# Kernel optimization log

Measured on AMD Instinct MI355X. Metric: run time of the kernel, lower is better.

The kernel has to match this reference:

```python
import jax, jax.numpy as jnp
import numpy as np
from jax import lax

ALPHA = 1.5
N_ITER = 100


def entmax(z, alpha=ALPHA, n_iter=N_ITER):
    # z: [B, Sq, Sk] scores. Bisection for the entmax threshold tau.
    z = (alpha - 1.0) * z.astype(jnp.float32)
    S = z.shape[-1]
    z_max = jnp.max(z, axis=-1, keepdims=True)          # [B, Sq, 1]
    tau_min = z_max - 1.0
    tau_max = z_max - np.float32(S ** (1.0 - alpha))
    inv = 1.0 / (alpha - 1.0)                            # = 2.0 for alpha=1.5

    def body(carry, _):
        tmin, tmax, _ = carry
        tau = (tmin + tmax) * 0.5
        p = jnp.maximum(z - tau, 0.0) ** inv             # [B, Sq, Sk]
        Z = jnp.sum(p, axis=-1, keepdims=True)           # [B, Sq, 1]
        tmin = jnp.where(Z >= 1.0, tau, tmin)
        tmax = jnp.where(Z < 1.0, tau, tmax)
        return (tmin, tmax, tau), None

    init = (tau_min, tau_max, (tau_min + tau_max) * 0.5)
    (tmin, tmax, tau), _ = lax.scan(jax.checkpoint(body), init, None, length=n_iter)
    # faithful to the TF code: final output uses p, Z from the LAST iteration's tau
    p = jnp.maximum(z - tau, 0.0) ** inv
    Z = jnp.sum(p, axis=-1, keepdims=True)
    return p / Z


def setup_inputs() -> dict:
    key = jax.random.key(0)
    kq, kk, kv = jax.random.split(key, 3)
    B, S, D = 8, 2048, 128
    return {
        "query": jax.random.normal(kq, (B, S, D), dtype=jnp.float32),
        "key": jax.random.normal(kk, (B, S, D), dtype=jnp.float32),
        "value": jax.random.normal(kv, (B, S, D), dtype=jnp.float32),
    }


def reference(query, key, value):
    scores = jnp.einsum("bqd,bkd->bqk", query, key)      # QK^T, no scaling (as in source)
    weights = entmax(scores, alpha=ALPHA, n_iter=N_ITER)
    return jnp.einsum("bqk,bkd->bqd", weights, value)
```

## Files before the change

kernel.cpp:

```cpp
#include <hip/hip_runtime.h>

#define BB 8
#define SS 2048
#define DD 128
#define ROWS 16
#define NW 8
#define CTW 16

typedef short bf16x8 __attribute__((ext_vector_type(8)));
typedef float f32x4 __attribute__((ext_vector_type(4)));

template <int I> struct IC { static constexpr int value = I; };
template <int I, int N, typename F>
__device__ __forceinline__ void sfor(F&& f) {
  if constexpr (I < N) { f(IC<I>{}); sfor<I + 1, N>((F&&)f); }
}

__device__ __forceinline__ short f2bf(float x) {
  return __builtin_bit_cast(short, (__bf16)x);
}
__device__ __forceinline__ float bf2f(short u) {
  return __uint_as_float(((unsigned)(unsigned short)u) << 16);
}
__device__ __forceinline__ unsigned pk2(float a, float b) {
  return (unsigned)(unsigned short)f2bf(a) |
         ((unsigned)(unsigned short)f2bf(b) << 16);
}

template <int N> __device__ __forceinline__ void wait_vm() {
  if constexpr (N >= 6)      asm volatile("s_waitcnt vmcnt(6)" ::: "memory");
  else if constexpr (N == 5) asm volatile("s_waitcnt vmcnt(5)" ::: "memory");
  else if constexpr (N == 4) asm volatile("s_waitcnt vmcnt(4)" ::: "memory");
  else if constexpr (N == 3) asm volatile("s_waitcnt vmcnt(3)" ::: "memory");
  else if constexpr (N == 2) asm volatile("s_waitcnt vmcnt(2)" ::: "memory");
  else if constexpr (N == 1) asm volatile("s_waitcnt vmcnt(1)" ::: "memory");
  else                       asm volatile("s_waitcnt vmcnt(0)" ::: "memory");
}

__device__ __forceinline__ void stage1(const short* g, short* l) {
  __builtin_amdgcn_global_load_lds(
      (const __attribute__((address_space(1))) void*)g,
      (__attribute__((address_space(3))) void*)l, 16, 0, 0);
}

__global__ __launch_bounds__(256)
void ksplit(const float* __restrict__ K, short* __restrict__ Khi) {
  const int lin  = blockIdx.x * 256 + threadIdx.x;
  const int b    = lin >> 15;
  const int rem  = lin & 32767;
  const int ct   = rem >> 8;
  const int s    = (rem >> 6) & 3;
  const int lane = rem & 63;
  const int quad = lane >> 4, m16 = lane & 15;
  const size_t elem = (size_t)(b * SS + ct * 16 + m16) * DD + s * 32 + quad * 8;
  const float4 v0 = *(const float4*)(K + elem);
  const float4 v1 = *(const float4*)(K + elem + 4);
  const float f[8] = {v0.x, v0.y, v0.z, v0.w, v1.x, v1.y, v1.z, v1.w};
  bf16x8 h;
#pragma unroll
  for (int e = 0; e < 8; ++e) h[e] = f2bf(f[e]);
  *(bf16x8*)(Khi + (size_t)lin * 8) = h;
}

__global__ __launch_bounds__(512) __attribute__((amdgpu_waves_per_eu(4)))
void attn(const float* __restrict__ Q, const short* __restrict__ Khi,
          const float* __restrict__ K, const float* __restrict__ V,
          float* __restrict__ Out) {
  __shared__ short kring[NW][8][512];
  __shared__ unsigned short Qs[ROWS][136];
  __shared__ float rbuf[ROWS][64];
  __shared__ int   scol[ROWS][64];
  __shared__ float exM[NW][ROWS];
  __shared__ int   rcnt[ROWS];
  __shared__ int   rovf[ROWS];
  __shared__ float tauB[ROWS], ZB[ROWS];

  const int tid  = threadIdx.x;
  const int lane = tid & 63;
  const int wid  = __builtin_amdgcn_readfirstlane(tid >> 6);
  const int quad = lane >> 4, m16 = lane & 15;
  const int b    = blockIdx.x & 7;
  const int qt   = blockIdx.x >> 3;

  const float* Qb = Q + (size_t)(b * SS + qt * ROWS) * DD;
  const float* Kb = K + (size_t)b * SS * DD;
  const float* Vb = V + (size_t)b * SS * DD;
  float*       Ob = Out + (size_t)(b * SS + qt * ROWS) * DD;
  const short* KHb = Khi + (size_t)b * SS * DD;

  if (tid < ROWS) { rcnt[tid] = 0; rovf[tid] = 0; }

  {
    const int row = tid >> 5, d = (tid & 31) * 4;
    const float4 v = *(const float4*)&Qb[row * DD + d];
    ushort4 h;
    h.x = (unsigned short)f2bf(0.5f * v.x);
    h.y = (unsigned short)f2bf(0.5f * v.y);
    h.z = (unsigned short)f2bf(0.5f * v.z);
    h.w = (unsigned short)f2bf(0.5f * v.w);
    *(ushort4*)&Qs[row][d] = h;
  }
  __syncthreads();

  bf16x8 qh[4];
#pragma unroll
  for (int s = 0; s < 4; ++s)
    qh[s] = *(const bf16x8*)&Qs[m16][s * 32 + quad * 8];

  short* ring = &kring[wid][0][0];
  const short* gw = KHb + ((size_t)(wid * CTW) << 11) + lane * 8;

  sfor<0, 7>([&](auto pc) {
    constexpr int p = pc.value;
    stage1(gw + p * 512, ring + p * 512);
  });

  unsigned zpk[CTW][2];
  float mx[4] = {-1e38f, -1e38f, -1e38f, -1e38f};
  f32x4 acc = {0.f, 0.f, 0.f, 0.f};

  sfor<0, 64>([&](auto qc) {
    constexpr int q = qc.value;
    wait_vm<(63 - q < 6 ? 63 - q : 6)>();
    asm volatile("s_waitcnt lgkmcnt(0)" ::: "memory");
    if constexpr (q + 7 < 64)
      stage1(gw + (q + 7) * 512, ring + ((q + 7) & 7) * 512);
    const bf16x8 bh = *(const bf16x8*)(ring + ((q & 7) << 9) + lane * 8);
    constexpr int s = q & 3;
    if constexpr (s == 0) acc = f32x4{0.f, 0.f, 0.f, 0.f};
    acc = __builtin_amdgcn_mfma_f32_16x16x32_bf16(qh[s], bh, acc, 0, 0, 0);
    if constexpr (s == 3) {
      constexpr int ct = q >> 2;
#pragma unroll
      for (int j = 0; j < 4; ++j) mx[j] = fmaxf(mx[j], acc[j]);
      zpk[ct][0] = pk2(acc[0], acc[1]);
      zpk[ct][1] = pk2(acc[2], acc[3]);
    }
  });

#pragma unroll
  for (int j = 0; j < 4; ++j)
#pragma unroll
    for (int s = 1; s <= 8; s <<= 1) mx[j] = fmaxf(mx[j], __shfl_xor(mx[j], s));
  if (m16 == 0) {
#pragma unroll
    for (int j = 0; j < 4; ++j) exM[wid][4 * quad + j] = mx[j];
  }
  __syncthreads();
  float M4[4];
#pragma unroll
  for (int j = 0; j < 4; ++j) {
    float m = -1e38f;
#pragma unroll
    for (int w = 0; w < NW; ++w) m = fmaxf(m, exM[w][4 * quad + j]);
    M4[j] = m;
  }

  sfor<0, CTW>([&](auto cc) {
    constexpr int ct = cc.value;
    const int col = wid * 256 + ct * 16 + m16;
    float v[4];
    v[0] = __uint_as_float(zpk[ct][0] << 16);
    v[1] = __uint_as_float(zpk[ct][0] & 0xffff0000u);
    v[2] = __uint_as_float(zpk[ct][1] << 16);
    v[3] = __uint_as_float(zpk[ct][1] & 0xffff0000u);
#pragma unroll
    for (int j = 0; j < 4; ++j) {
      const int row = 4 * quad + j;
      if (v[j] > M4[j] - 1.35f) {
        const int pos = atomicAdd(&rcnt[row], 1);
        if (pos < 64) { scol[row][pos] = col; rbuf[row][pos] = v[j]; }
        else rovf[row] = 1;
      }
    }
  });
  __syncthreads();

  const int rr32 = lane >> 5;
  const int row  = 2 * wid + rr32;
  const int l32  = lane & 31;
  const int nA = rcnt[2 * wid]     < 64 ? rcnt[2 * wid]     : 64;
  const int nB = rcnt[2 * wid + 1] < 64 ? rcnt[2 * wid + 1] : 64;
  const int nr  = rr32 ? nB : nA;
  const int nmx = nA > nB ? nA : nB;

  {
    const float4 q4 = *(const float4*)&Qb[row * DD + l32 * 4];
    for (int i = 0; i < nmx; ++i) {
      const bool act = i < nr;
      const int c = act ? scol[row][i] : scol[row][0];
      const float4 k4 = *(const float4*)&Kb[(size_t)c * DD + l32 * 4];
      float t = q4.x * k4.x + q4.y * k4.y + q4.z * k4.z + q4.w * k4.w;
#pragma unroll
      for (int s = 1; s <= 16; s <<= 1) t += __shfl_xor(t, s);
      if (act && l32 == 0) rbuf[row][i] = 0.5f * t;
    }
  }

  {
    const float a0 = (l32 < nr)      ? rbuf[row][l32]      : -1e38f;
    const float a1 = (l32 + 32 < nr) ? rbuf[row][l32 + 32] : -1e38f;
    float Mr = fmaxf(a0, a1);
#pragma unroll
    for (int s = 1; s <= 16; s <<= 1) Mr = fmaxf(Mr, __shfl_xor(Mr, s));
    float tmn = Mr - 1.0f, tmx = Mr - 0.022097086912079608f;
    float tau = 0.5f * (tmn + tmx), Zr = 0.f;
    for (int it = 0; it < 100; ++it) {
      tau = 0.5f * (tmn + tmx);
      const float t0 = fmaxf(a0 - tau, 0.f);
      const float t1 = fmaxf(a1 - tau, 0.f);
      float zp = fmaf(t0, t0, t1 * t1);
#pragma unroll
      for (int s = 1; s <= 16; s <<= 1) zp += __shfl_xor(zp, s);
      Zr = zp;
      const float nmn = (zp >= 1.f) ? tau : tmn;
      const float nmx = (zp >= 1.f) ? tmx : tau;
      const bool ch = (nmn != tmn) || (nmx != tmx);
      tmn = nmn; tmx = nmx;
      if (!__any(ch)) break;
    }
    if (l32 == 0) { tauB[row] = tau; ZB[row] = Zr; }
  }

  if (!rovf[row]) {
    const float tau = tauB[row];
    const float iz  = 1.0f / ZB[row];
    float4 o = {0.f, 0.f, 0.f, 0.f};
    for (int i = 0; i < nr; ++i) {
      const float rv = rbuf[row][i];
      const float tt = fmaxf(rv - tau, 0.f);
      const float pi = tt * tt * iz;
      const int   c  = scol[row][i];
      const float4 v4 = *(const float4*)&Vb[(size_t)c * DD + l32 * 4];
      o.x = fmaf(pi, v4.x, o.x);
      o.y = fmaf(pi, v4.y, o.y);
      o.z = fmaf(pi, v4.z, o.z);
      o.w = fmaf(pi, v4.w, o.w);
    }
    *(float4*)&Ob[row * DD + l32 * 4] = o;
  }

#pragma unroll
  for (int rr = 0; rr < 2; ++rr) {
    const int frow = 2 * wid + rr;
    if (!rovf[frow]) continue;
    float* zr = (float*)&kring[wid][0][0];
    for (int c0 = 0; c0 < 32; ++c0) {
      const int c = c0 * 64 + lane;
      const float* kp = &Kb[(size_t)c * DD];
      float t = 0.f;
      for (int d = 0; d < DD; d += 4) {
        const float4 qv = *(const float4*)&Qb[frow * DD + d];
        const float4 kv = *(const float4*)&kp[d];
        t = fmaf(qv.x, kv.x, t); t = fmaf(qv.y, kv.y, t);
        t = fmaf(qv.z, kv.z, t); t = fmaf(qv.w, kv.w, t);
      }
      zr[c] = 0.5f * t;
    }
    float Mr = -1e38f;
    for (int c0 = 0; c0 < 32; ++c0) Mr = fmaxf(Mr, zr[c0 * 64 + lane]);
#pragma unroll
    for (int s = 1; s <= 32; s <<= 1) Mr = fmaxf(Mr, __shfl_xor(Mr, s));
    float tmn = Mr - 1.0f, tmx = Mr - 0.022097086912079608f;
    float tau = 0.5f * (tmn + tmx), Zr = 0.f;
    for (int it = 0; it < 100; ++it) {
      tau = 0.5f * (tmn + tmx);
      float zp = 0.f;
      for (int c0 = 0; c0 < 32; ++c0) {
        const float tt = fmaxf(zr[c0 * 64 + lane] - tau, 0.f);
        zp = fmaf(tt, tt, zp);
      }
#pragma unroll
      for (int s = 1; s <= 32; s <<= 1) zp += __shfl_xor(zp, s);
      Zr = zp;
      const float nmn = (zp >= 1.f) ? tau : tmn;
      const float nmx = (zp >= 1.f) ? tmx : tau;
      const bool ch = (nmn != tmn) || (nmx != tmx);
      tmn = nmn; tmx = nmx;
      if (!__any(ch)) break;
    }
    const float iz = 1.0f / Zr;
    float2 o = {0.f, 0.f};
    for (int c = 0; c < SS; ++c) {
      const float tt = fmaxf(zr[c] - tau, 0.f);
      if (tt > 0.f) {
        const float pi = tt * tt * iz;
        const float2 v2 = *(const float2*)&Vb[(size_t)c * DD + lane * 2];
        o.x = fmaf(pi, v2.x, o.x);
        o.y = fmaf(pi, v2.y, o.y);
      }
    }
    *(float2*)&Ob[frow * DD + lane * 2] = o;
  }
}

extern "C" void kernel_launch(void* const* d_in, const int* in_sizes, int n_in,
                              void* d_out, int out_size, void* d_ws, size_t ws_size,
                              hipStream_t stream) {
  const float* Q = (const float*)d_in[0];
  const float* K = (const float*)d_in[1];
  const float* V = (const float*)d_in[2];
  float* out = (float*)d_out;
  short* Khi = (short*)d_ws;

  hipLaunchKernelGGL(ksplit, dim3(BB * SS * DD / (256 * 8)), dim3(256), 0, stream,
                     K, Khi);
  hipLaunchKernelGGL(attn, dim3(BB * (SS / ROWS)), dim3(512), 0, stream,
                     Q, Khi, K, V, out);
}
```

Before: 128.0 us.

## Process 32 query rows per block, reusing each staged K tile across two MFMA row groups

Doubles the query rows per block from 16 to 32, so each bf16 K tile staged into LDS feeds two MFMA accumulators (two 16-row groups). This halves both the K streaming traffic per output row and the number of blocks. The candidate buffer capacity drops from 64 to 48 per row and shares LDS with the Q staging buffer to limit shared-memory growth. The prefetch depth is also reduced. The trade-offs are fewer blocks for occupancy, more rows falling into the slow full-row overflow fallback, and a more serial per-wave post-processing loop.

```diff
diff --git a/kernel.cpp b/kernel.cpp
--- a/kernel.cpp
+++ b/kernel.cpp
@@ -3,9 +3,10 @@
 #define BB 8
 #define SS 2048
 #define DD 128
-#define ROWS 16
+#define ROWS 32
 #define NW 8
 #define CTW 16
+#define CAP 48
 
 typedef short bf16x8 __attribute__((ext_vector_type(8)));
 typedef float f32x4 __attribute__((ext_vector_type(4)));
@@ -18,9 +19,6 @@
 
 __device__ __forceinline__ short f2bf(float x) {
   return __builtin_bit_cast(short, (__bf16)x);
-}
-__device__ __forceinline__ float bf2f(short u) {
-  return __uint_as_float(((unsigned)(unsigned short)u) << 16);
 }
 __device__ __forceinline__ unsigned pk2(float a, float b) {
   return (unsigned)(unsigned short)f2bf(a) |
@@ -67,9 +65,10 @@
           const float* __restrict__ K, const float* __restrict__ V,
           float* __restrict__ Out) {
   __shared__ short kring[NW][8][512];
-  __shared__ unsigned short Qs[ROWS][136];
-  __shared__ float rbuf[ROWS][64];
-  __shared__ int   scol[ROWS][64];
+  __shared__ __align__(16) char ubuf[12288];
+  unsigned short (*Qs)[136] = (unsigned short (*)[136])ubuf;
+  float (*rbuf)[CAP] = (float (*)[CAP])ubuf;
+  int   (*scol)[CAP] = (int (*)[CAP])(ubuf + ROWS * CAP * 4);
   __shared__ float exM[NW][ROWS];
   __shared__ int   rcnt[ROWS];
   __shared__ int   rovf[ROWS];
@@ -91,158 +90,197 @@
   if (tid < ROWS) { rcnt[tid] = 0; rovf[tid] = 0; }
 
   {
-    const int row = tid >> 5, d = (tid & 31) * 4;
-    const float4 v = *(const float4*)&Qb[row * DD + d];
-    ushort4 h;
-    h.x = (unsigned short)f2bf(0.5f * v.x);
-    h.y = (unsigned short)f2bf(0.5f * v.y);
-    h.z = (unsigned short)f2bf(0.5f * v.z);
-    h.w = (unsigned short)f2bf(0.5f * v.w);
-    *(ushort4*)&Qs[row][d] = h;
+    const int row = tid >> 4, d = (tid & 15) * 8;
+    const float4 v0 = *(const float4*)&Qb[row * DD + d];
+    const float4 v1 = *(const float4*)&Qb[row * DD + d + 4];
+    ushort4 h0, h1;
+    h0.x = (unsigned short)f2bf(0.5f * v0.x);
+    h0.y = (unsigned short)f2bf(0.5f * v0.y);
+    h0.z = (unsigned short)f2bf(0.5f * v0.z);
+    h0.w = (unsigned short)f2bf(0.5f * v0.w);
+    h1.x = (unsigned short)f2bf(0.5f * v1.x);
+    h1.y = (unsigned short)f2bf(0.5f * v1.y);
+    h1.z = (unsigned short)f2bf(0.5f * v1.z);
+    h1.w = (unsigned short)f2bf(0.5f * v1.w);
+    *(ushort4*)&Qs[row][d]     = h0;
+    *(ushort4*)&Qs[row][d + 4] = h1;
   }
   __syncthreads();
 
-  bf16x8 qh[4];
-#pragma unroll
-  for (int s = 0; s < 4; ++s)
-    qh[s] = *(const bf16x8*)&Qs[m16][s * 32 + quad * 8];
-
   short* ring = &kring[wid][0][0];
   const short* gw = KHb + ((size_t)(wid * CTW) << 11) + lane * 8;
 
-  sfor<0, 7>([&](auto pc) {
+  sfor<0, 6>([&](auto pc) {
     constexpr int p = pc.value;
     stage1(gw + p * 512, ring + p * 512);
   });
 
-  unsigned zpk[CTW][2];
-  float mx[4] = {-1e38f, -1e38f, -1e38f, -1e38f};
-  f32x4 acc = {0.f, 0.f, 0.f, 0.f};
-
-  sfor<0, 64>([&](auto qc) {
-    constexpr int q = qc.value;
-    wait_vm<(63 - q < 6 ? 63 - q : 6)>();
+  bf16x8 qh[2][4];
+#pragma unroll
+  for (int g = 0; g < 2; ++g)
+#pragma unroll
+    for (int s = 0; s < 4; ++s)
+      qh[g][s] = *(const bf16x8*)&Qs[g * 16 + m16][s * 32 + quad * 8];
+
+  unsigned zpk[2][CTW][2];
+  float mx[2][4] = {{-1e38f, -1e38f, -1e38f, -1e38f},
+                    {-1e38f, -1e38f, -1e38f, -1e38f}};
+  f32x4 accA = {0.f, 0.f, 0.f, 0.f}, accB = {0.f, 0.f, 0.f, 0.f};
+
+  sfor<0, 32>([&](auto ii) {
+    constexpr int i = ii.value;
+    constexpr int left = 62 - 2 * i;
+    wait_vm<(left < 0 ? 0 : (left > 4 ? 4 : left))>();
     asm volatile("s_waitcnt lgkmcnt(0)" ::: "memory");
-    if constexpr (q + 7 < 64)
-      stage1(gw + (q + 7) * 512, ring + ((q + 7) & 7) * 512);
-    const bf16x8 bh = *(const bf16x8*)(ring + ((q & 7) << 9) + lane * 8);
-    constexpr int s = q & 3;
-    if constexpr (s == 0) acc = f32x4{0.f, 0.f, 0.f, 0.f};
-    acc = __builtin_amdgcn_mfma_f32_16x16x32_bf16(qh[s], bh, acc, 0, 0, 0);
-    if constexpr (s == 3) {
-      constexpr int ct = q >> 2;
-#pragma unroll
-      for (int j = 0; j < 4; ++j) mx[j] = fmaxf(mx[j], acc[j]);
-      zpk[ct][0] = pk2(acc[0], acc[1]);
-      zpk[ct][1] = pk2(acc[2], acc[3]);
+    if constexpr (2 * i + 7 < 64) {
+      stage1(gw + (2 * i + 6) * 512, ring + ((2 * i + 6) & 7) * 512);
+      stage1(gw + (2 * i + 7) * 512, ring + ((2 * i + 7) & 7) * 512);
+    }
+    const bf16x8 b0 = *(const bf16x8*)(ring + (((2 * i)     & 7) << 9) + lane * 8);
+    const bf16x8 b1 = *(const bf16x8*)(ring + (((2 * i + 1) & 7) << 9) + lane * 8);
+    constexpr int s0 = (2 * i) & 3;
+    constexpr int s1 = s0 + 1;
+    if constexpr (s0 == 0) {
+      accA = f32x4{0.f, 0.f, 0.f, 0.f};
+      accB = f32x4{0.f, 0.f, 0.f, 0.f};
+    }
+    accA = __builtin_amdgcn_mfma_f32_16x16x32_bf16(qh[0][s0], b0, accA, 0, 0, 0);
+    accB = __builtin_amdgcn_mfma_f32_16x16x32_bf16(qh[1][s0], b0, accB, 0, 0, 0);
+    accA = __builtin_amdgcn_mfma_f32_16x16x32_bf16(qh[0][s1], b1, accA, 0, 0, 0);
+    accB = __builtin_amdgcn_mfma_f32_16x16x32_bf16(qh[1][s1], b1, accB, 0, 0, 0);
+    if constexpr (s1 == 3) {
+      constexpr int ct = i >> 1;
+#pragma unroll
+      for (int j = 0; j < 4; ++j) {
+        mx[0][j] = fmaxf(mx[0][j], accA[j]);
+        mx[1][j] = fmaxf(mx[1][j], accB[j]);
+      }
+      zpk[0][ct][0] = pk2(accA[0], accA[1]);
+      zpk[0][ct][1] = pk2(accA[2], accA[3]);
+      zpk[1][ct][0] = pk2(accB[0], accB[1]);
+      zpk[1][ct][1] = pk2(accB[2], accB[3]);
     }
   });
 
 #pragma unroll
-  for (int j = 0; j < 4; ++j)
-#pragma unroll
-    for (int s = 1; s <= 8; s <<= 1) mx[j] = fmaxf(mx[j], __shfl_xor(mx[j], s));
+  for (int g = 0; g < 2; ++g)
+#pragma unroll
+    for (int j = 0; j < 4; ++j)
+#pragma unroll
+      for (int s = 1; s <= 8; s <<= 1)
+        mx[g][j] = fmaxf(mx[g][j], __shfl_xor(mx[g][j], s));
   if (m16 == 0) {
 #pragma unroll
-    for (int j = 0; j < 4; ++j) exM[wid][4 * quad + j] = mx[j];
+    for (int g = 0; g < 2; ++g)
+#pragma unroll
+      for (int j = 0; j < 4; ++j) exM[wid][g * 16 + 4 * quad + j] = mx[g][j];
   }
   __syncthreads();
-  float M4[4];
-#pragma unroll
-  for (int j = 0; j < 4; ++j) {
-    float m = -1e38f;
-#pragma unroll
-    for (int w = 0; w < NW; ++w) m = fmaxf(m, exM[w][4 * quad + j]);
-    M4[j] = m;
-  }
+  float M4[2][4];
+#pragma unroll
+  for (int g = 0; g < 2; ++g)
+#pragma unroll
+    for (int j = 0; j < 4; ++j) {
+      float m = -1e38f;
+#pragma unroll
+      for (int w = 0; w < NW; ++w) m = fmaxf(m, exM[w][g * 16 + 4 * quad + j]);
+      M4[g][j] = m;
+    }
 
   sfor<0, CTW>([&](auto cc) {
     constexpr int ct = cc.value;
     const int col = wid * 256 + ct * 16 + m16;
-    float v[4];
-    v[0] = __uint_as_float(zpk[ct][0] << 16);
-    v[1] = __uint_as_float(zpk[ct][0] & 0xffff0000u);
-    v[2] = __uint_as_float(zpk[ct][1] << 16);
-    v[3] = __uint_as_float(zpk[ct][1] & 0xffff0000u);
-#pragma unroll
-    for (int j = 0; j < 4; ++j) {
-      const int row = 4 * quad + j;
-      if (v[j] > M4[j] - 1.35f) {
-        const int pos = atomicAdd(&rcnt[row], 1);
-        if (pos < 64) { scol[row][pos] = col; rbuf[row][pos] = v[j]; }
-        else rovf[row] = 1;
+#pragma unroll
+    for (int g = 0; g < 2; ++g) {
+      float v[4];
+      v[0] = __uint_as_float(zpk[g][ct][0] << 16);
+      v[1] = __uint_as_float(zpk[g][ct][0] & 0xffff0000u);
+      v[2] = __uint_as_float(zpk[g][ct][1] << 16);
+      v[3] = __uint_as_float(zpk[g][ct][1] & 0xffff0000u);
+#pragma unroll
+      for (int j = 0; j < 4; ++j) {
+        const int row = g * 16 + 4 * quad + j;
+        if (v[j] > M4[g][j] - 1.35f) {
+          const int pos = atomicAdd(&rcnt[row], 1);
+          if (pos < CAP) { scol[row][pos] = col; rbuf[row][pos] = v[j]; }
+          else rovf[row] = 1;
+        }
       }
     }
   });
   __syncthreads();
 
   const int rr32 = lane >> 5;
-  const int row  = 2 * wid + rr32;
   const int l32  = lane & 31;
-  const int nA = rcnt[2 * wid]     < 64 ? rcnt[2 * wid]     : 64;
-  const int nB = rcnt[2 * wid + 1] < 64 ? rcnt[2 * wid + 1] : 64;
-  const int nr  = rr32 ? nB : nA;
-  const int nmx = nA > nB ? nA : nB;
-
-  {
-    const float4 q4 = *(const float4*)&Qb[row * DD + l32 * 4];
-    for (int i = 0; i < nmx; ++i) {
-      const bool act = i < nr;
-      const int c = act ? scol[row][i] : scol[row][0];
-      const float4 k4 = *(const float4*)&Kb[(size_t)c * DD + l32 * 4];
-      float t = q4.x * k4.x + q4.y * k4.y + q4.z * k4.z + q4.w * k4.w;
-#pragma unroll
-      for (int s = 1; s <= 16; s <<= 1) t += __shfl_xor(t, s);
-      if (act && l32 == 0) rbuf[row][i] = 0.5f * t;
+
+#pragma unroll
+  for (int p = 0; p < 2; ++p) {
+    const int row = 4 * wid + 2 * p + rr32;
+    const int nA = rcnt[4 * wid + 2 * p]     < CAP ? rcnt[4 * wid + 2 * p]     : CAP;
+    const int nB = rcnt[4 * wid + 2 * p + 1] < CAP ? rcnt[4 * wid + 2 * p + 1] : CAP;
+    const int nr  = rr32 ? nB : nA;
+    const int nmx = nA > nB ? nA : nB;
+
+    {
+      const float4 q4 = *(const float4*)&Qb[row * DD + l32 * 4];
+      for (int i = 0; i < nmx; ++i) {
+        const bool act = i < nr;
+        const int c = act ? scol[row][i] : scol[row][0];
+        const float4 k4 = *(const float4*)&Kb[(size_t)c * DD + l32 * 4];
+        float t = q4.x * k4.x + q4.y * k4.y + q4.z * k4.z + q4.w * k4.w;
+#pragma unroll
+        for (int s = 1; s <= 16; s <<= 1) t += __shfl_xor(t, s);
+        if (act && l32 == 0) rbuf[row][i] = 0.5f * t;
+      }
+    }
+
+    {
+      const float a0 = (l32 < nr)      ? rbuf[row][l32]      : -1e38f;
+      const float a1 = (l32 + 32 < nr) ? rbuf[row][l32 + 32] : -1e38f;
+      float Mr = fmaxf(a0, a1);
+#pragma unroll
+      for (int s = 1; s <= 16; s <<= 1) Mr = fmaxf(Mr, __shfl_xor(Mr, s));
+      float tmn = Mr - 1.0f, tmx = Mr - 0.022097086912079608f;
+      float tau = 0.5f * (tmn + tmx), Zr = 0.f;
+      for (int it = 0; it < 100; ++it) {
+        tau = 0.5f * (tmn + tmx);
+        const float t0 = fmaxf(a0 - tau, 0.f);
+        const float t1 = fmaxf(a1 - tau, 0.f);
+        float zp = fmaf(t0, t0, t1 * t1);
+#pragma unroll
+        for (int s = 1; s <= 16; s <<= 1) zp += __shfl_xor(zp, s);
+        Zr = zp;
+        const float nmn = (zp >= 1.f) ? tau : tmn;
+        const float nmx2 = (zp >= 1.f) ? tmx : tau;
+        const bool ch = (nmn != tmn) || (nmx2 != tmx);
+        tmn = nmn; tmx = nmx2;
+        if (!__any(ch)) break;
+      }
+      if (l32 == 0) { tauB[row] = tau; ZB[row] = Zr; }
+    }
+
+    if (!rovf[row]) {
+      const float tau = tauB[row];
+      const float iz  = 1.0f / ZB[row];
+      float4 o = {0.f, 0.f, 0.f, 0.f};
+      for (int i = 0; i < nr; ++i) {
+        const float rv = rbuf[row][i];
+        const float tt = fmaxf(rv - tau, 0.f);
+        const float pi = tt * tt * iz;
+        const int   c  = scol[row][i];
+        const float4 v4 = *(const float4*)&Vb[(size_t)c * DD + l32 * 4];
+        o.x = fmaf(pi, v4.x, o.x);
+        o.y = fmaf(pi, v4.y, o.y);
+        o.z = fmaf(pi, v4.z, o.z);
+        o.w = fmaf(pi, v4.w, o.w);
+      }
+      *(float4*)&Ob[row * DD + l32 * 4] = o;
     }
   }
 
-  {
-    const float a0 = (l32 < nr)      ? rbuf[row][l32]      : -1e38f;
-    const float a1 = (l32 + 32 < nr) ? rbuf[row][l32 + 32] : -1e38f;
-    float Mr = fmaxf(a0, a1);
-#pragma unroll
-    for (int s = 1; s <= 16; s <<= 1) Mr = fmaxf(Mr, __shfl_xor(Mr, s));
-    float tmn = Mr - 1.0f, tmx = Mr - 0.022097086912079608f;
-    float tau = 0.5f * (tmn + tmx), Zr = 0.f;
-    for (int it = 0; it < 100; ++it) {
-      tau = 0.5f * (tmn + tmx);
-      const float t0 = fmaxf(a0 - tau, 0.f);
-      const float t1 = fmaxf(a1 - tau, 0.f);
-      float zp = fmaf(t0, t0, t1 * t1);
-#pragma unroll
-      for (int s = 1; s <= 16; s <<= 1) zp += __shfl_xor(zp, s);
-      Zr = zp;
-      const float nmn = (zp >= 1.f) ? tau : tmn;
-      const float nmx = (zp >= 1.f) ? tmx : tau;
-      const bool ch = (nmn != tmn) || (nmx != tmx);
-      tmn = nmn; tmx = nmx;
-      if (!__any(ch)) break;
-    }
-    if (l32 == 0) { tauB[row] = tau; ZB[row] = Zr; }
-  }
-
-  if (!rovf[row]) {
-    const float tau = tauB[row];
-    const float iz  = 1.0f / ZB[row];
-    float4 o = {0.f, 0.f, 0.f, 0.f};
-    for (int i = 0; i < nr; ++i) {
-      const float rv = rbuf[row][i];
-      const float tt = fmaxf(rv - tau, 0.f);
-      const float pi = tt * tt * iz;
-      const int   c  = scol[row][i];
-      const float4 v4 = *(const float4*)&Vb[(size_t)c * DD + l32 * 4];
-      o.x = fmaf(pi, v4.x, o.x);
-      o.y = fmaf(pi, v4.y, o.y);
-      o.z = fmaf(pi, v4.z, o.z);
-      o.w = fmaf(pi, v4.w, o.w);
-    }
-    *(float4*)&Ob[row * DD + l32 * 4] = o;
-  }
-
-#pragma unroll
-  for (int rr = 0; rr < 2; ++rr) {
-    const int frow = 2 * wid + rr;
+#pragma unroll
+  for (int rr = 0; rr < 4; ++rr) {
+    const int frow = 4 * wid + rr;
     if (!rovf[frow]) continue;
     float* zr = (float*)&kring[wid][0][0];
     for (int c0 = 0; c0 < 32; ++c0) {
@@ -274,9 +312,9 @@
       for (int s = 1; s <= 32; s <<= 1) zp += __shfl_xor(zp, s);
       Zr = zp;
       const float nmn = (zp >= 1.f) ? tau : tmn;
-      const float nmx = (zp >= 1.f) ? tmx : tau;
-      const bool ch = (nmn != tmn) || (nmx != tmx);
-      tmn = nmn; tmx = nmx;
+      const float nmx2 = (zp >= 1.f) ? tmx : tau;
+      const bool ch = (nmn != tmn) || (nmx2 != tmx);
+      tmn = nmn; tmx = nmx2;
       if (!__any(ch)) break;
     }
     const float iz = 1.0f / Zr;
```

Measured after the change: 152.9 us. 19.5% more time.

## Split attention into screening and tail kernels with global candidate lists

Applied to the files above, without the earlier changes.

Splits the fused attention kernel in two. A screening kernel writes candidate column indices per row into a global buffer using global atomics. A separate tail kernel with small 256-thread blocks does the exact rescoring, bisection and V accumulation, and also handles overflow rows with a block-cooperative full-row fallback. The candidate cap drops from 64 to 24, and the counters are zeroed inside ksplit. This is meant to relieve the large screening kernel of the serial tail work and to spread the tail across more blocks, at the cost of an extra launch, global-memory round trips and more rows falling back to the expensive path.

```diff
diff --git a/kernel.cpp b/kernel.cpp
--- a/kernel.cpp
+++ b/kernel.cpp
@@ -6,6 +6,7 @@
 #define ROWS 16
 #define NW 8
 #define CTW 16
+#define CAP 24
 
 typedef short bf16x8 __attribute__((ext_vector_type(8)));
 typedef float f32x4 __attribute__((ext_vector_type(4)));
@@ -18,9 +19,6 @@
 
 __device__ __forceinline__ short f2bf(float x) {
   return __builtin_bit_cast(short, (__bf16)x);
-}
-__device__ __forceinline__ float bf2f(short u) {
-  return __uint_as_float(((unsigned)(unsigned short)u) << 16);
 }
 __device__ __forceinline__ unsigned pk2(float a, float b) {
   return (unsigned)(unsigned short)f2bf(a) |
@@ -44,8 +42,10 @@
 }
 
 __global__ __launch_bounds__(256)
-void ksplit(const float* __restrict__ K, short* __restrict__ Khi) {
+void ksplit(const float* __restrict__ K, short* __restrict__ Khi,
+            int* __restrict__ cnt) {
   const int lin  = blockIdx.x * 256 + threadIdx.x;
+  if (lin < BB * SS) cnt[lin] = 0;
   const int b    = lin >> 15;
   const int rem  = lin & 32767;
   const int ct   = rem >> 8;
@@ -63,17 +63,11 @@
 }
 
 __global__ __launch_bounds__(512) __attribute__((amdgpu_waves_per_eu(4)))
-void attn(const float* __restrict__ Q, const short* __restrict__ Khi,
-          const float* __restrict__ K, const float* __restrict__ V,
-          float* __restrict__ Out) {
+void screen(const float* __restrict__ Q, const short* __restrict__ Khi,
+            int* __restrict__ candC, int* __restrict__ cnt) {
   __shared__ short kring[NW][8][512];
   __shared__ unsigned short Qs[ROWS][136];
-  __shared__ float rbuf[ROWS][64];
-  __shared__ int   scol[ROWS][64];
   __shared__ float exM[NW][ROWS];
-  __shared__ int   rcnt[ROWS];
-  __shared__ int   rovf[ROWS];
-  __shared__ float tauB[ROWS], ZB[ROWS];
 
   const int tid  = threadIdx.x;
   const int lane = tid & 63;
@@ -81,14 +75,10 @@
   const int quad = lane >> 4, m16 = lane & 15;
   const int b    = blockIdx.x & 7;
   const int qt   = blockIdx.x >> 3;
-
-  const float* Qb = Q + (size_t)(b * SS + qt * ROWS) * DD;
-  const float* Kb = K + (size_t)b * SS * DD;
-  const float* Vb = V + (size_t)b * SS * DD;
-  float*       Ob = Out + (size_t)(b * SS + qt * ROWS) * DD;
+  const int rowBase = b * SS + qt * ROWS;
+
+  const float* Qb = Q + (size_t)rowBase * DD;
   const short* KHb = Khi + (size_t)b * SS * DD;
-
-  if (tid < ROWS) { rcnt[tid] = 0; rovf[tid] = 0; }
 
   {
     const int row = tid >> 5, d = (tid & 31) * 4;
@@ -166,131 +156,155 @@
     v[3] = __uint_as_float(zpk[ct][1] & 0xffff0000u);
 #pragma unroll
     for (int j = 0; j < 4; ++j) {
-      const int row = 4 * quad + j;
       if (v[j] > M4[j] - 1.35f) {
-        const int pos = atomicAdd(&rcnt[row], 1);
-        if (pos < 64) { scol[row][pos] = col; rbuf[row][pos] = v[j]; }
-        else rovf[row] = 1;
+        const int rowg = rowBase + 4 * quad + j;
+        const int pos = atomicAdd(&cnt[rowg], 1);
+        if (pos < CAP) candC[rowg * CAP + pos] = col;
       }
     }
   });
+}
+
+__global__ __launch_bounds__(256)
+void tail(const float* __restrict__ Q, const float* __restrict__ K,
+          const float* __restrict__ V, const int* __restrict__ candC,
+          const int* __restrict__ cnt, float* __restrict__ Out) {
+  __shared__ float zv[4][2][CAP];
+  __shared__ float zscr[SS];
+  __shared__ int   ovfs[8];
+  __shared__ float ftau, fZ;
+
+  const int tid  = threadIdx.x;
+  const int w    = tid >> 6;
+  const int lane = tid & 63;
+  const int rr32 = lane >> 5, l32 = lane & 31;
+  const int rowgA = blockIdx.x * 8 + w * 2;
+  const int rowg  = rowgA + rr32;
+  const int b     = rowg >> 11;
+
+  if (tid < 8) ovfs[tid] = 0;
   __syncthreads();
 
-  const int rr32 = lane >> 5;
-  const int row  = 2 * wid + rr32;
-  const int l32  = lane & 31;
-  const int nA = rcnt[2 * wid]     < 64 ? rcnt[2 * wid]     : 64;
-  const int nB = rcnt[2 * wid + 1] < 64 ? rcnt[2 * wid + 1] : 64;
-  const int nr  = rr32 ? nB : nA;
-  const int nmx = nA > nB ? nA : nB;
+  const int nrawA = cnt[rowgA], nrawB = cnt[rowgA + 1];
+  const int nA = nrawA < CAP ? nrawA : CAP;
+  const int nB = nrawB < CAP ? nrawB : CAP;
+  const int nr   = rr32 ? nB : nA;
+  const int nmx  = nA > nB ? nA : nB;
+  const bool ovf = (rr32 ? nrawB : nrawA) > CAP;
+
+  const float* Qg = Q + (size_t)rowg * DD;
+  const float* Kb = K + (size_t)b * SS * DD;
+  const float* Vb = V + (size_t)b * SS * DD;
 
   {
-    const float4 q4 = *(const float4*)&Qb[row * DD + l32 * 4];
+    const float4 q4 = *(const float4*)&Qg[l32 * 4];
     for (int i = 0; i < nmx; ++i) {
       const bool act = i < nr;
-      const int c = act ? scol[row][i] : scol[row][0];
+      const int c = candC[rowg * CAP + (act ? i : 0)];
       const float4 k4 = *(const float4*)&Kb[(size_t)c * DD + l32 * 4];
       float t = q4.x * k4.x + q4.y * k4.y + q4.z * k4.z + q4.w * k4.w;
 #pragma unroll
       for (int s = 1; s <= 16; s <<= 1) t += __shfl_xor(t, s);
-      if (act && l32 == 0) rbuf[row][i] = 0.5f * t;
-    }
-  }
-
+      if (act && l32 == 0) zv[w][rr32][i] = 0.5f * t;
+    }
+  }
+
+  float tau, Zr = 0.f;
   {
-    const float a0 = (l32 < nr)      ? rbuf[row][l32]      : -1e38f;
-    const float a1 = (l32 + 32 < nr) ? rbuf[row][l32 + 32] : -1e38f;
-    float Mr = fmaxf(a0, a1);
+    const float a0 = (l32 < nr) ? zv[w][rr32][l32] : -1e38f;
+    float Mr = a0;
 #pragma unroll
     for (int s = 1; s <= 16; s <<= 1) Mr = fmaxf(Mr, __shfl_xor(Mr, s));
     float tmn = Mr - 1.0f, tmx = Mr - 0.022097086912079608f;
-    float tau = 0.5f * (tmn + tmx), Zr = 0.f;
+    tau = 0.5f * (tmn + tmx);
     for (int it = 0; it < 100; ++it) {
       tau = 0.5f * (tmn + tmx);
       const float t0 = fmaxf(a0 - tau, 0.f);
-      const float t1 = fmaxf(a1 - tau, 0.f);
-      float zp = fmaf(t0, t0, t1 * t1);
+      float zp = t0 * t0;
 #pragma unroll
       for (int s = 1; s <= 16; s <<= 1) zp += __shfl_xor(zp, s);
       Zr = zp;
       const float nmn = (zp >= 1.f) ? tau : tmn;
-      const float nmx = (zp >= 1.f) ? tmx : tau;
-      const bool ch = (nmn != tmn) || (nmx != tmx);
-      tmn = nmn; tmx = nmx;
+      const float nmx2 = (zp >= 1.f) ? tmx : tau;
+      const bool ch = (nmn != tmn) || (nmx2 != tmx);
+      tmn = nmn; tmx = nmx2;
       if (!__any(ch)) break;
     }
-    if (l32 == 0) { tauB[row] = tau; ZB[row] = Zr; }
-  }
-
-  if (!rovf[row]) {
-    const float tau = tauB[row];
-    const float iz  = 1.0f / ZB[row];
+  }
+
+  if (!ovf) {
+    const float iz = 1.0f / Zr;
     float4 o = {0.f, 0.f, 0.f, 0.f};
     for (int i = 0; i < nr; ++i) {
-      const float rv = rbuf[row][i];
-      const float tt = fmaxf(rv - tau, 0.f);
+      const float tt = fmaxf(zv[w][rr32][i] - tau, 0.f);
       const float pi = tt * tt * iz;
-      const int   c  = scol[row][i];
+      const int   c  = candC[rowg * CAP + i];
       const float4 v4 = *(const float4*)&Vb[(size_t)c * DD + l32 * 4];
       o.x = fmaf(pi, v4.x, o.x);
       o.y = fmaf(pi, v4.y, o.y);
       o.z = fmaf(pi, v4.z, o.z);
       o.w = fmaf(pi, v4.w, o.w);
     }
-    *(float4*)&Ob[row * DD + l32 * 4] = o;
-  }
-
-#pragma unroll
-  for (int rr = 0; rr < 2; ++rr) {
-    const int frow = 2 * wid + rr;
-    if (!rovf[frow]) continue;
-    float* zr = (float*)&kring[wid][0][0];
-    for (int c0 = 0; c0 < 32; ++c0) {
-      const int c = c0 * 64 + lane;
-      const float* kp = &Kb[(size_t)c * DD];
+    *(float4*)&Out[(size_t)rowg * DD + l32 * 4] = o;
+  } else if (l32 == 0) {
+    ovfs[w * 2 + rr32] = 1;
+  }
+  __syncthreads();
+
+  for (int r8 = 0; r8 < 8; ++r8) {
+    if (!ovfs[r8]) continue;
+    const int fr = blockIdx.x * 8 + r8;
+    const int fb = fr >> 11;
+    const float* fQ = Q + (size_t)fr * DD;
+    const float* fK = K + (size_t)fb * SS * DD;
+    const float* fV = V + (size_t)fb * SS * DD;
+    for (int c = tid; c < SS; c += 256) {
       float t = 0.f;
       for (int d = 0; d < DD; d += 4) {
-        const float4 qv = *(const float4*)&Qb[frow * DD + d];
-        const float4 kv = *(const float4*)&kp[d];
+        const float4 qv = *(const float4*)&fQ[d];
+        const float4 kv = *(const float4*)&fK[(size_t)c * DD + d];
         t = fmaf(qv.x, kv.x, t); t = fmaf(qv.y, kv.y, t);
         t = fmaf(qv.z, kv.z, t); t = fmaf(qv.w, kv.w, t);
       }
-      zr[c] = 0.5f * t;
-    }
-    float Mr = -1e38f;
-    for (int c0 = 0; c0 < 32; ++c0) Mr = fmaxf(Mr, zr[c0 * 64 + lane]);
-#pragma unroll
-    for (int s = 1; s <= 32; s <<= 1) Mr = fmaxf(Mr, __shfl_xor(Mr, s));
-    float tmn = Mr - 1.0f, tmx = Mr - 0.022097086912079608f;
-    float tau = 0.5f * (tmn + tmx), Zr = 0.f;
-    for (int it = 0; it < 100; ++it) {
-      tau = 0.5f * (tmn + tmx);
-      float zp = 0.f;
-      for (int c0 = 0; c0 < 32; ++c0) {
-        const float tt = fmaxf(zr[c0 * 64 + lane] - tau, 0.f);
-        zp = fmaf(tt, tt, zp);
+      zscr[c] = 0.5f * t;
+    }
+    __syncthreads();
+    if (w == 0) {
+      float Mr = -1e38f;
+      for (int c0 = 0; c0 < 32; ++c0) Mr = fmaxf(Mr, zscr[c0 * 64 + lane]);
+#pragma unroll
+      for (int s = 1; s <= 32; s <<= 1) Mr = fmaxf(Mr, __shfl_xor(Mr, s));
+      float tmn = Mr - 1.0f, tmx = Mr - 0.022097086912079608f;
+      float ta = 0.5f * (tmn + tmx), Zf = 0.f;
+      for (int it = 0; it < 100; ++it) {
+        ta = 0.5f * (tmn + tmx);
+        float zp = 0.f;
+        for (int c0 = 0; c0 < 32; ++c0) {
+          const float tt = fmaxf(zscr[c0 * 64 + lane] - ta, 0.f);
+          zp = fmaf(tt, tt, zp);
+        }
+#pragma unroll
+        for (int s = 1; s <= 32; s <<= 1) zp += __shfl_xor(zp, s);
+        Zf = zp;
+        const float nmn = (zp >= 1.f) ? ta : tmn;
+        const float nmx2 = (zp >= 1.f) ? tmx : ta;
+        const bool ch = (nmn != tmn) || (nmx2 != tmx);
+        tmn = nmn; tmx = nmx2;
+        if (!__any(ch)) break;
       }
-#pragma unroll
-      for (int s = 1; s <= 32; s <<= 1) zp += __shfl_xor(zp, s);
-      Zr = zp;
-      const float nmn = (zp >= 1.f) ? tau : tmn;
-      const float nmx = (zp >= 1.f) ? tmx : tau;
-      const bool ch = (nmn != tmn) || (nmx != tmx);
-      tmn = nmn; tmx = nmx;
-      if (!__any(ch)) break;
-    }
-    const float iz = 1.0f / Zr;
-    float2 o = {0.f, 0.f};
-    for (int c = 0; c < SS; ++c) {
-      const float tt = fmaxf(zr[c] - tau, 0.f);
-      if (tt > 0.f) {
-        const float pi = tt * tt * iz;
-        const float2 v2 = *(const float2*)&Vb[(size_t)c * DD + lane * 2];
-        o.x = fmaf(pi, v2.x, o.x);
-        o.y = fmaf(pi, v2.y, o.y);
+      if (lane == 0) { ftau = ta; fZ = Zf; }
+    }
+    __syncthreads();
+    if (tid < DD) {
+      const float ta = ftau, iz = 1.0f / fZ;
+      float o = 0.f;
+      for (int c = 0; c < SS; ++c) {
+        const float tt = fmaxf(zscr[c] - ta, 0.f);
+        if (tt > 0.f) o = fmaf(tt * tt * iz, fV[(size_t)c * DD + tid], o);
       }
-    }
-    *(float2*)&Ob[frow * DD + lane * 2] = o;
+      Out[(size_t)fr * DD + tid] = o;
+    }
+    __syncthreads();
   }
 }
 
@@ -301,10 +315,14 @@
   const float* K = (const float*)d_in[1];
   const float* V = (const float*)d_in[2];
   float* out = (float*)d_out;
-  short* Khi = (short*)d_ws;
+  short* Khi  = (short*)d_ws;
+  int*   candC = (int*)((char*)d_ws + (size_t)BB * SS * DD * 2);
+  int*   cnt   = candC + (size_t)BB * SS * CAP;
 
   hipLaunchKernelGGL(ksplit, dim3(BB * SS * DD / (256 * 8)), dim3(256), 0, stream,
-                     K, Khi);
-  hipLaunchKernelGGL(attn, dim3(BB * (SS / ROWS)), dim3(512), 0, stream,
-                     Q, Khi, K, V, out);
-}
+                     K, Khi, cnt);
+  hipLaunchKernelGGL(screen, dim3(BB * (SS / ROWS)), dim3(512), 0, stream,
+                     Q, Khi, candC, cnt);
+  hipLaunchKernelGGL(tail, dim3(BB * SS / 8), dim3(256), 0, stream,
+                     Q, K, V, candC, cnt, out);
+}
```

Result: slower. 141.0 us (+10.2%).

## Double-buffer whole K tiles and keep fp32 scores in registers for selection

Applied to the files above, without the earlier changes.

The ksplit kernel now reads K fully coalesced and scatters each chunk to the MFMA-ready layout on the store side instead of the load side. The attention kernel drops the 8-slot per-step ring and double-buffers whole 16-column K tiles (4 loads each), with a vmcnt(4) wait per tile rather than per step. The 16 fp32 score accumulators stay in registers instead of being packed to bf16, and the candidate threshold is tightened from 1.35 to 1.25 so fewer entries reach the sparse path. Costs are higher register pressure (waves_per_eu relaxed to 3–4) and less load lookahead; the tighter threshold relies on the fp32 scores being exact enough to avoid missing support entries.

```diff
diff --git a/kernel.cpp b/kernel.cpp
--- a/kernel.cpp
+++ b/kernel.cpp
@@ -19,54 +19,39 @@
 __device__ __forceinline__ short f2bf(float x) {
   return __builtin_bit_cast(short, (__bf16)x);
 }
-__device__ __forceinline__ float bf2f(short u) {
-  return __uint_as_float(((unsigned)(unsigned short)u) << 16);
-}
-__device__ __forceinline__ unsigned pk2(float a, float b) {
-  return (unsigned)(unsigned short)f2bf(a) |
-         ((unsigned)(unsigned short)f2bf(b) << 16);
-}
-
-template <int N> __device__ __forceinline__ void wait_vm() {
-  if constexpr (N >= 6)      asm volatile("s_waitcnt vmcnt(6)" ::: "memory");
-  else if constexpr (N == 5) asm volatile("s_waitcnt vmcnt(5)" ::: "memory");
-  else if constexpr (N == 4) asm volatile("s_waitcnt vmcnt(4)" ::: "memory");
-  else if constexpr (N == 3) asm volatile("s_waitcnt vmcnt(3)" ::: "memory");
-  else if constexpr (N == 2) asm volatile("s_waitcnt vmcnt(2)" ::: "memory");
-  else if constexpr (N == 1) asm volatile("s_waitcnt vmcnt(1)" ::: "memory");
-  else                       asm volatile("s_waitcnt vmcnt(0)" ::: "memory");
-}
-
-__device__ __forceinline__ void stage1(const short* g, short* l) {
-  __builtin_amdgcn_global_load_lds(
-      (const __attribute__((address_space(1))) void*)g,
-      (__attribute__((address_space(3))) void*)l, 16, 0, 0);
+
+__device__ __forceinline__ void stage_tile(const short* g, short* l) {
+#pragma unroll
+  for (int s = 0; s < 4; ++s) {
+    __builtin_amdgcn_global_load_lds(
+        (const __attribute__((address_space(1))) void*)(g + (s << 9)),
+        (__attribute__((address_space(3))) void*)(l + (s << 9)), 16, 0, 0);
+  }
 }
 
 __global__ __launch_bounds__(256)
 void ksplit(const float* __restrict__ K, short* __restrict__ Khi) {
-  const int lin  = blockIdx.x * 256 + threadIdx.x;
-  const int b    = lin >> 15;
-  const int rem  = lin & 32767;
-  const int ct   = rem >> 8;
-  const int s    = (rem >> 6) & 3;
-  const int lane = rem & 63;
-  const int quad = lane >> 4, m16 = lane & 15;
-  const size_t elem = (size_t)(b * SS + ct * 16 + m16) * DD + s * 32 + quad * 8;
-  const float4 v0 = *(const float4*)(K + elem);
-  const float4 v1 = *(const float4*)(K + elem + 4);
-  const float f[8] = {v0.x, v0.y, v0.z, v0.w, v1.x, v1.y, v1.z, v1.w};
+  const int lin = blockIdx.x * 256 + threadIdx.x;
+  const int r   = lin >> 4;
+  const int c8  = lin & 15;
+  const float4 v0 = *(const float4*)(K + (size_t)lin * 8);
+  const float4 v1 = *(const float4*)(K + (size_t)lin * 8 + 4);
   bf16x8 h;
-#pragma unroll
-  for (int e = 0; e < 8; ++e) h[e] = f2bf(f[e]);
-  *(bf16x8*)(Khi + (size_t)lin * 8) = h;
-}
-
-__global__ __launch_bounds__(512) __attribute__((amdgpu_waves_per_eu(4)))
+  h[0] = f2bf(v0.x); h[1] = f2bf(v0.y); h[2] = f2bf(v0.z); h[3] = f2bf(v0.w);
+  h[4] = f2bf(v1.x); h[5] = f2bf(v1.y); h[6] = f2bf(v1.z); h[7] = f2bf(v1.w);
+  const int bct  = r >> 4;
+  const int m16  = r & 15;
+  const int s    = c8 >> 2;
+  const int quad = c8 & 3;
+  const size_t out = ((((size_t)bct * 4 + s) * 64) + quad * 16 + m16) * 8;
+  *(bf16x8*)(Khi + out) = h;
+}
+
+__global__ __launch_bounds__(512) __attribute__((amdgpu_waves_per_eu(3, 4)))
 void attn(const float* __restrict__ Q, const short* __restrict__ Khi,
           const float* __restrict__ K, const float* __restrict__ V,
           float* __restrict__ Out) {
-  __shared__ short kring[NW][8][512];
+  __shared__ short kring[NW][2][2048];
   __shared__ unsigned short Qs[ROWS][136];
   __shared__ float rbuf[ROWS][64];
   __shared__ int   scol[ROWS][64];
@@ -107,37 +92,37 @@
   for (int s = 0; s < 4; ++s)
     qh[s] = *(const bf16x8*)&Qs[m16][s * 32 + quad * 8];
 
-  short* ring = &kring[wid][0][0];
+  short* ring0 = &kring[wid][0][0];
+  short* ring1 = &kring[wid][1][0];
   const short* gw = KHb + ((size_t)(wid * CTW) << 11) + lane * 8;
 
-  sfor<0, 7>([&](auto pc) {
-    constexpr int p = pc.value;
-    stage1(gw + p * 512, ring + p * 512);
+  stage_tile(gw + 0 * 2048, ring0);
+  stage_tile(gw + 1 * 2048, ring1);
+
+  f32x4 acc[CTW];
+  sfor<0, CTW>([&](auto ic) {
+    constexpr int i = ic.value;
+    if constexpr (i < CTW - 1) asm volatile("s_waitcnt vmcnt(4)" ::: "memory");
+    else                       asm volatile("s_waitcnt vmcnt(0)" ::: "memory");
+    const short* sbl = ((i & 1) ? ring1 : ring0) + lane * 8;
+    f32x4 c = {0.f, 0.f, 0.f, 0.f};
+    sfor<0, 4>([&](auto sc) {
+      constexpr int s = sc.value;
+      const bf16x8 bh = *(const bf16x8*)(sbl + (s << 9));
+      c = __builtin_amdgcn_mfma_f32_16x16x32_bf16(qh[s], bh, c, 0, 0, 0);
+    });
+    acc[i] = c;
+    if constexpr (i + 2 < CTW) {
+      asm volatile("s_waitcnt lgkmcnt(0)" ::: "memory");
+      stage_tile(gw + (i + 2) * 2048, (i & 1) ? ring1 : ring0);
+    }
   });
 
-  unsigned zpk[CTW][2];
   float mx[4] = {-1e38f, -1e38f, -1e38f, -1e38f};
-  f32x4 acc = {0.f, 0.f, 0.f, 0.f};
-
-  sfor<0, 64>([&](auto qc) {
-    constexpr int q = qc.value;
-    wait_vm<(63 - q < 6 ? 63 - q : 6)>();
-    asm volatile("s_waitcnt lgkmcnt(0)" ::: "memory");
-    if constexpr (q + 7 < 64)
-      stage1(gw + (q + 7) * 512, ring + ((q + 7) & 7) * 512);
-    const bf16x8 bh = *(const bf16x8*)(ring + ((q & 7) << 9) + lane * 8);
-    constexpr int s = q & 3;
-    if constexpr (s == 0) acc = f32x4{0.f, 0.f, 0.f, 0.f};
-    acc = __builtin_amdgcn_mfma_f32_16x16x32_bf16(qh[s], bh, acc, 0, 0, 0);
-    if constexpr (s == 3) {
-      constexpr int ct = q >> 2;
-#pragma unroll
-      for (int j = 0; j < 4; ++j) mx[j] = fmaxf(mx[j], acc[j]);
-      zpk[ct][0] = pk2(acc[0], acc[1]);
-      zpk[ct][1] = pk2(acc[2], acc[3]);
-    }
+  sfor<0, CTW>([&](auto ic) {
+#pragma unroll
+    for (int j = 0; j < 4; ++j) mx[j] = fmaxf(mx[j], acc[ic.value][j]);
   });
-
 #pragma unroll
   for (int j = 0; j < 4; ++j)
 #pragma unroll
@@ -156,20 +141,15 @@
     M4[j] = m;
   }
 
-  sfor<0, CTW>([&](auto cc) {
-    constexpr int ct = cc.value;
-    const int col = wid * 256 + ct * 16 + m16;
-    float v[4];
-    v[0] = __uint_as_float(zpk[ct][0] << 16);
-    v[1] = __uint_as_float(zpk[ct][0] & 0xffff0000u);
-    v[2] = __uint_as_float(zpk[ct][1] << 16);
-    v[3] = __uint_as_float(zpk[ct][1] & 0xffff0000u);
+  sfor<0, CTW>([&](auto ic) {
+    constexpr int i = ic.value;
+    const int col = wid * 256 + i * 16 + m16;
 #pragma unroll
     for (int j = 0; j < 4; ++j) {
       const int row = 4 * quad + j;
-      if (v[j] > M4[j] - 1.35f) {
+      if (acc[i][j] > M4[j] - 1.25f) {
         const int pos = atomicAdd(&rcnt[row], 1);
-        if (pos < 64) { scol[row][pos] = col; rbuf[row][pos] = v[j]; }
+        if (pos < 64) { scol[row][pos] = col; rbuf[row][pos] = acc[i][j]; }
         else rovf[row] = 1;
       }
     }
@@ -214,9 +194,9 @@
       for (int s = 1; s <= 16; s <<= 1) zp += __shfl_xor(zp, s);
       Zr = zp;
       const float nmn = (zp >= 1.f) ? tau : tmn;
-      const float nmx = (zp >= 1.f) ? tmx : tau;
-      const bool ch = (nmn != tmn) || (nmx != tmx);
-      tmn = nmn; tmx = nmx;
+      const float nmx2 = (zp >= 1.f) ? tmx : tau;
+      const bool ch = (nmn != tmn) || (nmx2 != tmx);
+      tmn = nmn; tmx = nmx2;
       if (!__any(ch)) break;
     }
     if (l32 == 0) { tauB[row] = tau; ZB[row] = Zr; }
@@ -274,9 +254,9 @@
       for (int s = 1; s <= 32; s <<= 1) zp += __shfl_xor(zp, s);
       Zr = zp;
       const float nmn = (zp >= 1.f) ? tau : tmn;
-      const float nmx = (zp >= 1.f) ? tmx : tau;
-      const bool ch = (nmn != tmn) || (nmx != tmx);
-      tmn = nmn; tmx = nmx;
+      const float nmx2 = (zp >= 1.f) ? tmx : tau;
+      const bool ch = (nmn != tmn) || (nmx2 != tmx);
+      tmn = nmn; tmx = nmx2;
       if (!__any(ch)) break;
     }
     const float iz = 1.0f / Zr;
```

Result: no change. 127.2 us (-0.6%).
